# Performance work log

Measured on AMD Instinct MI355X. Metric: run time of the kernel, lower is better.

Reference implementation:

```python
import jax, jax.numpy as jnp
import numpy as np


def _hadamard_mats():
    r1 = np.array([[1,0,0,0,1,0,0,0],[0,1,0,0,0,1,0,0],[0,0,1,0,0,0,1,0],[0,0,0,1,0,0,0,1],[1,0,0,0,-1,0,0,0],[0,1,0,0,0,-1,0,0],[0,0,1,0,0,0,-1,0],[0,0,0,1,0,0,0,-1]], dtype=np.float32)
    r2 = np.array([[1,0,1,0,0,0,0,0],[0,1,0,1,0,0,0,0],[1,0,-1,0,0,0,0,0],[0,1,0,-1,0,0,0,0],[0,0,0,0,1,0,1,0],[0,0,0,0,0,1,0,1],[0,0,0,0,1,0,-1,0],[0,0,0,0,0,1,0,-1]], dtype=np.float32)
    r3 = np.array([[1,1,0,0,0,0,0,0],[1,-1,0,0,0,0,0,0],[0,0,1,1,0,0,0,0],[0,0,1,-1,0,0,0,0],[0,0,0,0,1,1,0,0],[0,0,0,0,1,-1,0,0],[0,0,0,0,0,0,1,1],[0,0,0,0,0,0,1,-1]], dtype=np.float32)
    lmul = r1.T @ r2.T @ r3.T  # l1.dot(l2).dot(l3)
    rmul = r1 @ r2 @ r3
    return jnp.asarray(lmul), jnp.asarray(rmul)


def setup_inputs() -> dict:
    key = jax.random.key(0)
    k1, k2 = jax.random.split(key)
    B, C, H, W = 16, 3, 512, 512
    inp = jax.random.normal(k1, (B, C, H, W), dtype=jnp.float32)
    lab = jax.random.normal(k2, (B, C, H, W), dtype=jnp.float32)
    lmul, rmul = _hadamard_mats()
    return {"input": inp, "label": lab, "lmul": lmul, "rmul": rmul}


def reference(input, label, lmul, rmul):
    B, C, H, W = input.shape
    diff = input - label
    # split into non-overlapping 8x8 blocks: [B, C, H//8, 8, W//8, 8]
    d = diff.reshape(B, C, H // 8, 8, W // 8, 8)
    # per-block: lmul @ block @ rmul
    t = jnp.einsum('ij,bchjwk,kl->bchiwl', lmul, d, rmul)
    return jnp.mean(jnp.abs(t))
```

## Files before the change

kernel.cpp:

```cpp
#include <hip/hip_runtime.h>


#define N_TOTAL ((float)(16LL * 3 * 512 * 512))
#define PHYS_WAVES 6144
#define UPW 4
#define GRID1 1536

__device__ __forceinline__ void fht8(float* x) {
#pragma unroll
    for (int s = 4; s >= 1; s >>= 1) {
#pragma unroll
        for (int i = 0; i < 8; ++i) {
            if ((i & s) == 0) {
                float u = x[i], w = x[i + s];
                x[i] = u + w;
                x[i + s] = u - w;
            }
        }
    }
}

__global__ __launch_bounds__(256) void satd_partial(const float* __restrict__ a,
                                                    const float* __restrict__ b,
                                                    float* __restrict__ ws) {
    int lane = threadIdx.x & 63;
    int wid  = threadIdx.x >> 6;
    int pw   = blockIdx.x * 4 + wid;
    int sub  = lane & 7;
    int r    = lane >> 3;

    float s_ = 0.0f;
#pragma unroll
    for (int u = 0; u < UPW; ++u) {
        int w   = pw + u * PHYS_WAVES;
        int wx  = w & 7;
        int by  = (w >> 3) & 63;
        int img = w >> 9;

        size_t base = ((size_t)img * 512 + (size_t)(by * 8 + r)) * 512
                    + (size_t)(wx * 8 + sub) * 8;

        const float4* pa = reinterpret_cast<const float4*>(a + base);
        const float4* pb = reinterpret_cast<const float4*>(b + base);
        float4 a0 = pa[0], a1 = pa[1];
        float4 b0 = pb[0], b1 = pb[1];
        float x[8] = {a0.x - b0.x, a0.y - b0.y, a0.z - b0.z, a0.w - b0.w,
                      a1.x - b1.x, a1.y - b1.y, a1.z - b1.z, a1.w - b1.w};

        fht8(x);

#pragma unroll
        for (int s = 4; s >= 1; s >>= 1) {
            int mask = s << 3;
            bool up = (lane & mask) == 0;
#pragma unroll
            for (int c = 0; c < 8; ++c) {
                float p = __shfl_xor(x[c], mask);
                x[c] = up ? (x[c] + p) : (p - x[c]);
            }
        }

#pragma unroll
        for (int c = 0; c < 8; ++c) s_ += fabsf(x[c]);
    }

#pragma unroll
    for (int off = 32; off >= 1; off >>= 1) s_ += __shfl_down(s_, off);

    __shared__ float red[4];
    if (lane == 0) red[wid] = s_;
    __syncthreads();
    if (threadIdx.x == 0)
        ws[blockIdx.x] = red[0] + red[1] + red[2] + red[3];
}

__global__ __launch_bounds__(256) void satd_final(const float* __restrict__ ws,
                                                  float* __restrict__ out) {
    int t = threadIdx.x;
    float s_ = 0.0f;
#pragma unroll
    for (int k = 0; k < GRID1 / 256; ++k) s_ += ws[t + 256 * k];

#pragma unroll
    for (int off = 32; off >= 1; off >>= 1) s_ += __shfl_down(s_, off);

    __shared__ float red[4];
    int lane = t & 63, wid = t >> 6;
    if (lane == 0) red[wid] = s_;
    __syncthreads();
    if (t == 0)
        out[0] = (red[0] + red[1] + red[2] + red[3]) * (1.0f / N_TOTAL);
}

extern "C" void kernel_launch(void* const* d_in, const int* in_sizes, int n_in,
                              void* d_out, int out_size, void* d_ws, size_t ws_size,
                              hipStream_t stream) {
    const float* a = (const float*)d_in[0];
    const float* b = (const float*)d_in[1];
    float* out = (float*)d_out;
    float* ws  = (float*)d_ws;

    satd_partial<<<dim3(GRID1), dim3(256), 0, stream>>>(a, b, ws);
    satd_final<<<dim3(1), dim3(256), 0, stream>>>(ws, out);
}
```

Baseline: 22.56 us.

## Remap work so each lane holds a column strip of a block row set

Each wave now covers 8 rows by 256 columns of one image; each lane loads one float4 per row for 8 rows of a and b, so all 16 loads are issued up front. The column transform is now one xor-1 shuffle plus an in-register 4-point butterfly, and the row transform runs entirely in registers. This replaces the 3-stage cross-lane shuffle over 8 values per unit with one shuffle stage per value, and gives each row load fully contiguous 1 KB wave accesses. It trades this for higher per-thread register pressure from 16 float4 live values, and each wave does the same total work as before with no inner loop.

```diff
diff --git a/kernel.cpp b/kernel.cpp
--- a/kernel.cpp
+++ b/kernel.cpp
@@ -2,73 +2,73 @@
 
 
 #define N_TOTAL ((float)(16LL * 3 * 512 * 512))
-#define PHYS_WAVES 6144
-#define UPW 4
 #define GRID1 1536
-
-__device__ __forceinline__ void fht8(float* x) {
-#pragma unroll
-    for (int s = 4; s >= 1; s >>= 1) {
-#pragma unroll
-        for (int i = 0; i < 8; ++i) {
-            if ((i & s) == 0) {
-                float u = x[i], w = x[i + s];
-                x[i] = u + w;
-                x[i + s] = u - w;
-            }
-        }
-    }
-}
 
 __global__ __launch_bounds__(256) void satd_partial(const float* __restrict__ a,
                                                     const float* __restrict__ b,
                                                     float* __restrict__ ws) {
-    int lane = threadIdx.x & 63;
-    int wid  = threadIdx.x >> 6;
-    int pw   = blockIdx.x * 4 + wid;
-    int sub  = lane & 7;
-    int r    = lane >> 3;
+    const int lane = threadIdx.x & 63;
+    const int wid  = threadIdx.x >> 6;
+    const int s    = blockIdx.x * 4 + wid;
+    const int xh   = s & 1;
+    const int y8   = (s >> 1) & 63;
+    const int img  = s >> 7;
 
-    float s_ = 0.0f;
+    const size_t base = (size_t)img * (512 * 512)
+                      + (size_t)(y8 * 8) * 512 + (size_t)(xh * 256) + (lane << 2);
+
+    float4 av[8], bv[8];
 #pragma unroll
-    for (int u = 0; u < UPW; ++u) {
-        int w   = pw + u * PHYS_WAVES;
-        int wx  = w & 7;
-        int by  = (w >> 3) & 63;
-        int img = w >> 9;
+    for (int i = 0; i < 8; ++i)
+        av[i] = *reinterpret_cast<const float4*>(a + base + (size_t)(i * 512));
+#pragma unroll
+    for (int i = 0; i < 8; ++i)
+        bv[i] = *reinterpret_cast<const float4*>(b + base + (size_t)(i * 512));
 
-        size_t base = ((size_t)img * 512 + (size_t)(by * 8 + r)) * 512
-                    + (size_t)(wx * 8 + sub) * 8;
+    float v[8][4];
+#pragma unroll
+    for (int r = 0; r < 8; ++r) {
+        v[r][0] = av[r].x - bv[r].x;
+        v[r][1] = av[r].y - bv[r].y;
+        v[r][2] = av[r].z - bv[r].z;
+        v[r][3] = av[r].w - bv[r].w;
+    }
 
-        const float4* pa = reinterpret_cast<const float4*>(a + base);
-        const float4* pb = reinterpret_cast<const float4*>(b + base);
-        float4 a0 = pa[0], a1 = pa[1];
-        float4 b0 = pb[0], b1 = pb[1];
-        float x[8] = {a0.x - b0.x, a0.y - b0.y, a0.z - b0.z, a0.w - b0.w,
-                      a1.x - b1.x, a1.y - b1.y, a1.z - b1.z, a1.w - b1.w};
-
-        fht8(x);
-
+    const float sx = (lane & 1) ? -1.0f : 1.0f;
 #pragma unroll
-        for (int s = 4; s >= 1; s >>= 1) {
-            int mask = s << 3;
-            bool up = (lane & mask) == 0;
+    for (int r = 0; r < 8; ++r)
 #pragma unroll
-            for (int c = 0; c < 8; ++c) {
-                float p = __shfl_xor(x[c], mask);
-                x[c] = up ? (x[c] + p) : (p - x[c]);
-            }
+        for (int c = 0; c < 4; ++c) {
+            float p = __shfl_xor(v[r][c], 1);
+            v[r][c] = fmaf(sx, v[r][c], p);
         }
 
 #pragma unroll
-        for (int c = 0; c < 8; ++c) s_ += fabsf(x[c]);
+    for (int r = 0; r < 8; ++r) {
+        float u0 = v[r][0], u1 = v[r][1], u2 = v[r][2], u3 = v[r][3];
+        float t0 = u0 + u2, t2 = u0 - u2, t1 = u1 + u3, t3 = u1 - u3;
+        v[r][0] = t0 + t1; v[r][1] = t0 - t1;
+        v[r][2] = t2 + t3; v[r][3] = t2 - t3;
+    }
+
+    float acc = 0.0f;
+#pragma unroll
+    for (int c = 0; c < 4; ++c) {
+        float x0 = v[0][c], x1 = v[1][c], x2 = v[2][c], x3 = v[3][c];
+        float x4 = v[4][c], x5 = v[5][c], x6 = v[6][c], x7 = v[7][c];
+        float y0 = x0 + x4, y4 = x0 - x4, y1 = x1 + x5, y5 = x1 - x5;
+        float y2 = x2 + x6, y6 = x2 - x6, y3 = x3 + x7, y7 = x3 - x7;
+        float z0 = y0 + y2, z2 = y0 - y2, z1 = y1 + y3, z3 = y1 - y3;
+        float z4 = y4 + y6, z6 = y4 - y6, z5 = y5 + y7, z7 = y5 - y7;
+        acc += fabsf(z0 + z1) + fabsf(z0 - z1) + fabsf(z2 + z3) + fabsf(z2 - z3)
+             + fabsf(z4 + z5) + fabsf(z4 - z5) + fabsf(z6 + z7) + fabsf(z6 - z7);
     }
 
 #pragma unroll
-    for (int off = 32; off >= 1; off >>= 1) s_ += __shfl_down(s_, off);
+    for (int off = 32; off >= 1; off >>= 1) acc += __shfl_down(acc, off);
 
     __shared__ float red[4];
-    if (lane == 0) red[wid] = s_;
+    if (lane == 0) red[wid] = acc;
     __syncthreads();
     if (threadIdx.x == 0)
         ws[blockIdx.x] = red[0] + red[1] + red[2] + red[3];
```

Measured after the change: 22.12 us. About the same (-2.0%).
